# Kernel optimization log

Measured on AMD Instinct MI355X. Metric: run time of the kernel, lower is better.

## Reference

```python
import jax, jax.numpy as jnp
import numpy as np

NPOINT = 2048
RADIUS = 0.1
NSAMPLE = 32


def fps(xyz, npoint):
    # Furthest point sampling, deterministic start at index 0 (matches pointnet2_utils).
    B, N, _ = xyz.shape
    dist0 = jnp.full((B, N), 1e10, dtype=xyz.dtype)
    far0 = jnp.zeros((B,), dtype=jnp.int32)

    def step(carry, _):
        dist, far = carry
        centroid = jnp.take_along_axis(xyz, far[:, None, None], axis=1)  # (B,1,3)
        d = jnp.sum((xyz - centroid) ** 2, axis=-1)                      # (B,N)
        dist = jnp.minimum(dist, d)
        new_far = jnp.argmax(dist, axis=-1).astype(jnp.int32)
        return (dist, new_far), far

    _, idx = jax.lax.scan(step, (dist0, far0), None, length=npoint)
    return idx.T  # (B, npoint)


def ball_query(xyz, new_xyz, radius, nsample):
    # For each center, indices of up to nsample points within radius (pad with first hit).
    N = xyz.shape[1]
    sqr = jnp.sum((new_xyz[:, :, None, :] - xyz[:, None, :, :]) ** 2, axis=-1)  # (B,S,N)
    cand = jnp.where(sqr <= radius * radius, jnp.arange(N, dtype=jnp.int32), N)
    cand = jnp.sort(cand, axis=-1)[:, :, :nsample]  # (B,S,K)
    first = cand[:, :, :1]
    first = jnp.where(first == N, 0, first)
    return jnp.where(cand == N, first, cand)


def batched_gather(points, idx):
    # points (B,N,C), idx (B,...) -> (B,...,C)
    return jax.vmap(lambda p, i: p[i])(points, idx)


def reference(xyz, features, W0, b0, W1, b1, W2, b2):
    # xyz: (B,N,3), features: (B,C,N)
    fps_idx = fps(xyz, NPOINT)                                  # (B,S)
    new_xyz = batched_gather(xyz, fps_idx)                      # (B,S,3)
    idx = ball_query(xyz, new_xyz, RADIUS, NSAMPLE)             # (B,S,K)

    grouped_xyz = batched_gather(xyz, idx) - new_xyz[:, :, None, :]   # (B,S,K,3) relative coords
    grouped_feat = batched_gather(features.transpose(0, 2, 1), idx)   # (B,S,K,C)
    grouped = jnp.concatenate([grouped_xyz, grouped_feat], axis=-1)   # (B,S,K,C+3)
    x = grouped.transpose(0, 3, 1, 2)                                 # (B,C+3,S,K)

    # SharedMLP: 1x1 conv2d + ReLU stack
    x = jax.nn.relu(jnp.einsum('oi,bisk->bosk', W0, x) + b0[None, :, None, None])
    x = jax.nn.relu(jnp.einsum('oi,bisk->bosk', W1, x) + b1[None, :, None, None])
    x = jax.nn.relu(jnp.einsum('oi,bisk->bosk', W2, x) + b2[None, :, None, None])

    new_features = jnp.max(x, axis=-1)  # max-pool over nsample -> (B,128,S)
    return new_xyz, new_features


def setup_inputs() -> dict:
    key = jax.random.key(0)
    ks = jax.random.split(key, 8)
    B, N, C = 4, 8192, 64
    s = 0.05  # keep activations in a sane range through 3 relu layers
    return {
        'xyz': jax.random.uniform(ks[0], (B, N, 3), dtype=jnp.float32),
        'features': jax.random.normal(ks[1], (B, C, N), dtype=jnp.float32),
        'W0': jax.random.normal(ks[2], (64, 67), dtype=jnp.float32) * s,
        'b0': jax.random.normal(ks[3], (64,), dtype=jnp.float32) * s,
        'W1': jax.random.normal(ks[4], (64, 64), dtype=jnp.float32) * s,
        'b1': jax.random.normal(ks[5], (64,), dtype=jnp.float32) * s,
        'W2': jax.random.normal(ks[6], (128, 64), dtype=jnp.float32) * s,
        'b2': jax.random.normal(ks[7], (128,), dtype=jnp.float32) * s,
    }
```

## Files before the change

### kernel.cpp

```cpp
#include <hip/hip_runtime.h>

#define NB 4
#define NPTS 8192
#define NPOINT 2048
#define NSAMPLE 32
#define CF 64
#define CIN 67
#define G 8

typedef float f32x2 __attribute__((ext_vector_type(2)));
typedef unsigned long long u64;

__device__ __forceinline__ f32x2 pk_add(f32x2 a, f32x2 b) {
  f32x2 d;
  asm("v_pk_add_f32 %0, %1, %2" : "=v"(d) : "v"(a), "v"(b));
  return d;
}
__device__ __forceinline__ f32x2 pk_mul(f32x2 a, f32x2 b) {
  f32x2 d;
  asm("v_pk_mul_f32 %0, %1, %2" : "=v"(d) : "v"(a), "v"(b));
  return d;
}

template <int CTRL, int RM>
__device__ __forceinline__ int dppi(int v) {
  return __builtin_amdgcn_update_dpp(0, v, CTRL, RM, 0xf, true);
}
template <int CTRL, int RM>
__device__ __forceinline__ u64 kstep(u64 k) {
  unsigned lo = (unsigned)k, hi = (unsigned)(k >> 32);
  unsigned olo = (unsigned)dppi<CTRL, RM>((int)lo);
  unsigned ohi = (unsigned)dppi<CTRL, RM>((int)hi);
  u64 o = ((u64)ohi << 32) | olo;
  return o > k ? o : k;
}
__device__ __forceinline__ u64 wave_max_key(u64 key) {
  key = kstep<0x111, 0xf>(key);
  key = kstep<0x112, 0xf>(key);
  key = kstep<0x114, 0xf>(key);
  key = kstep<0x118, 0xf>(key);
  key = kstep<0x142, 0xa>(key);
  key = kstep<0x143, 0xc>(key);
  return key;
}
__device__ __forceinline__ unsigned wave_scan_incl(unsigned v) {
  v += (unsigned)__builtin_amdgcn_update_dpp(0, (int)v, 0x111, 0xf, 0xf, true);
  v += (unsigned)__builtin_amdgcn_update_dpp(0, (int)v, 0x112, 0xf, 0xf, true);
  v += (unsigned)__builtin_amdgcn_update_dpp(0, (int)v, 0x114, 0xf, 0xf, true);
  v += (unsigned)__builtin_amdgcn_update_dpp(0, (int)v, 0x118, 0xf, 0xf, true);
  v += (unsigned)__builtin_amdgcn_update_dpp(0, (int)v, 0x142, 0xa, 0xf, true);
  v += (unsigned)__builtin_amdgcn_update_dpp(0, (int)v, 0x143, 0xc, 0xf, true);
  return v;
}

__device__ __forceinline__ int cellof(float x) {
  int c = (int)(x * 8.0f);
  return c > 7 ? 7 : (c < 0 ? 0 : c);
}
__device__ __forceinline__ unsigned morton9(int ix, int iy, int iz) {
  unsigned m = 0;
#pragma unroll
  for (int k = 0; k < 3; ++k) {
    m |= ((unsigned)((ix >> k) & 1) << (3 * k + 2)) |
         ((unsigned)((iy >> k) & 1) << (3 * k + 1)) |
         ((unsigned)((iz >> k) & 1) << (3 * k + 0));
  }
  return m;
}

__global__ __launch_bounds__(512) void fps_kernel(const float* __restrict__ xyz,
                                                  float* __restrict__ new_xyz) {
  const int b = blockIdx.x;
  const int tid = threadIdx.x;
  const int lane = tid & 63;
  const int wid = tid >> 6;
  __shared__ float sx[NPTS], sy[NPTS], sz[NPTS];
  __shared__ unsigned sidx[NPTS];
  __shared__ unsigned offs[512];
  __shared__ unsigned wsum[8];
  __shared__ int farhist[NPOINT];
  __shared__ __align__(16) u64 skey[2][8];

  const float* xb = xyz + (size_t)b * NPTS * 3;
  for (int i = tid; i < NPTS; i += 512) {
    sx[i] = xb[3 * i + 0];
    sy[i] = xb[3 * i + 1];
    sz[i] = xb[3 * i + 2];
  }
  offs[tid] = 0;
  __syncthreads();
  for (int r = 0; r < 16; ++r) {
    int i = tid + r * 512;
    unsigned m = morton9(cellof(sx[i]), cellof(sy[i]), cellof(sz[i]));
    atomicAdd(&offs[m], 1u);
  }
  __syncthreads();
  unsigned v = offs[tid];
  unsigned inc = wave_scan_incl(v);
  if (lane == 63) wsum[wid] = inc;
  __syncthreads();
  unsigned pre = 0;
#pragma unroll
  for (int w = 0; w < 8; ++w) pre += (w < wid) ? wsum[w] : 0u;
  unsigned excl = pre + inc - v;
  __syncthreads();
  offs[tid] = excl;
  __syncthreads();
  for (int r = 0; r < 16; ++r) {
    int i = tid + r * 512;
    unsigned m = morton9(cellof(sx[i]), cellof(sy[i]), cellof(sz[i]));
    unsigned pos = atomicAdd(&offs[m], 1u);
    sidx[pos] = (unsigned)i;
  }
  __syncthreads();

  f32x2 px[8], py[8], pz[8];
  float dist[16];
  unsigned noid[16];
  float blx = 1e30f, bhx = -1e30f, bly = 1e30f, bhy = -1e30f,
        blz = 1e30f, bhz = -1e30f;
#pragma unroll
  for (int j = 0; j < 8; ++j) {
    unsigned i0 = sidx[tid * 16 + 2 * j], i1 = sidx[tid * 16 + 2 * j + 1];
    noid[2 * j] = ~i0; noid[2 * j + 1] = ~i1;
    float x0 = sx[i0], x1 = sx[i1];
    float y0 = sy[i0], y1 = sy[i1];
    float z0 = sz[i0], z1 = sz[i1];
    px[j].x = x0; px[j].y = x1;
    py[j].x = y0; py[j].y = y1;
    pz[j].x = z0; pz[j].y = z1;
    blx = fminf(blx, fminf(x0, x1)); bhx = fmaxf(bhx, fmaxf(x0, x1));
    bly = fminf(bly, fminf(y0, y1)); bhy = fmaxf(bhy, fmaxf(y0, y1));
    blz = fminf(blz, fminf(z0, z1)); bhz = fmaxf(bhz, fmaxf(z0, z1));
    dist[2 * j] = 1e10f; dist[2 * j + 1] = 1e10f;
  }
  float gmaxd = 1e30f;
  u64 gkey = 0;
  int far = 0;
  for (int it = 0; it < NPOINT; ++it) {
    if (tid == 0) farhist[it] = far;
    const float cx = sx[far], cy = sy[far], cz = sz[far];
    float gx = fmaxf(fmaxf(blx - cx, cx - bhx), 0.f);
    float gy = fmaxf(fmaxf(bly - cy, cy - bhy), 0.f);
    float gz = fmaxf(fmaxf(blz - cz, cz - bhz), 0.f);
    float mind2 = gx * gx + gy * gy + gz * gz;
    if (mind2 * 0.999f < gmaxd) {
      f32x2 ncx, ncy, ncz;
      ncx.x = -cx; ncx.y = -cx;
      ncy.x = -cy; ncy.y = -cy;
      ncz.x = -cz; ncz.y = -cz;
      u64 k = 0;
#pragma unroll
      for (int j = 0; j < 8; ++j) {
        f32x2 dx = pk_add(px[j], ncx);
        f32x2 dy = pk_add(py[j], ncy);
        f32x2 dz = pk_add(pz[j], ncz);
        f32x2 xx = pk_mul(dx, dx);
        f32x2 yy = pk_mul(dy, dy);
        f32x2 dd = pk_add(pk_add(xx, yy), pk_mul(dz, dz));
        float n0 = fminf(dist[2 * j], dd.x);
        float n1 = fminf(dist[2 * j + 1], dd.y);
        dist[2 * j] = n0; dist[2 * j + 1] = n1;
        u64 k0 = ((u64)__float_as_uint(n0) << 32) | noid[2 * j];
        k = k0 > k ? k0 : k;
        u64 k1 = ((u64)__float_as_uint(n1) << 32) | noid[2 * j + 1];
        k = k1 > k ? k1 : k;
      }
      gkey = k;
      gmaxd = __uint_as_float((unsigned)(k >> 32));
    }
    u64 key = wave_max_key(gkey);
    const int p = it & 1;
    if (lane == 63) skey[p][wid] = key;
    __syncthreads();
    const ulonglong2* kp = (const ulonglong2*)&skey[p][0];
    ulonglong2 k0 = kp[0], k1 = kp[1], k2 = kp[2], k3 = kp[3];
    u64 m0 = k0.x > k0.y ? k0.x : k0.y;
    u64 m1 = k1.x > k1.y ? k1.x : k1.y;
    u64 m2 = k2.x > k2.y ? k2.x : k2.y;
    u64 m3 = k3.x > k3.y ? k3.x : k3.y;
    u64 m4 = m0 > m1 ? m0 : m1;
    u64 m5 = m2 > m3 ? m2 : m3;
    u64 best = m4 > m5 ? m4 : m5;
    far = (int)~(unsigned)best;
  }
  __syncthreads();
  for (int t = tid; t < NPOINT; t += 512) {
    int f = farhist[t];
    float* o = new_xyz + ((size_t)b * NPOINT + t) * 3;
    o[0] = sx[f]; o[1] = sy[f]; o[2] = sz[f];
  }
}

__global__ __launch_bounds__(256) void tr_kernel(const float* __restrict__ f,
                                                 float* __restrict__ ft) {
  int idx = blockIdx.x * 256 + threadIdx.x;
  int c = idx & 63;
  int i = (idx >> 6) & (NPTS - 1);
  int b = idx >> 19;
  ft[idx] = f[((size_t)(b * CF + c)) * NPTS + i];
}

__global__ __launch_bounds__(256) void bq_kernel(const float* __restrict__ xyz,
                                                 const float* __restrict__ new_xyz,
                                                 int* __restrict__ idxbuf) {
  const int lane = threadIdx.x & 63;
  const int gw = (blockIdx.x * 256 + threadIdx.x) >> 6;
  const int b = gw >> 11;
  const int j = gw & 2047;
  const float* xb = xyz + (size_t)b * NPTS * 3;
  const float* c = new_xyz + ((size_t)b * NPOINT + j) * 3;
  const float cx = c[0], cy = c[1], cz = c[2];
  int* out = idxbuf + ((size_t)b * NPOINT + j) * NSAMPLE;
  const float r2 = 0.01f;
  int found = 0, first = 0;
  for (int base = 0; base < NPTS && found < NSAMPLE; base += 64) {
    const int i = base + lane;
    float dx = xb[3 * i + 0] - cx, dy = xb[3 * i + 1] - cy, dz = xb[3 * i + 2] - cz;
    float d = __fadd_rn(__fadd_rn(__fmul_rn(dx, dx), __fmul_rn(dy, dy)),
                        __fmul_rn(dz, dz));
    bool in = (d <= r2);
    unsigned long long mask = __ballot(in);
    if (mask) {
      if (found == 0) first = base + (__ffsll(mask) - 1);
      int slot = found + __popcll(mask & ((1ull << lane) - 1ull));
      if (in && slot < NSAMPLE) out[slot] = i;
      found += (int)__popcll(mask);
    }
  }
  for (int s = found + lane; s < NSAMPLE; s += 64) out[s] = first;
}

__global__ __launch_bounds__(256) void mlp_kernel(const float* __restrict__ xyz,
                                                  const float* __restrict__ ft,
                                                  const float* __restrict__ feat,
                                                  const int* __restrict__ idxbuf,
                                                  const float* __restrict__ new_xyz,
                                                  const float* __restrict__ W0,
                                                  const float* __restrict__ b0,
                                                  const float* __restrict__ W1,
                                                  const float* __restrict__ b1,
                                                  const float* __restrict__ W2,
                                                  const float* __restrict__ b2,
                                                  float* __restrict__ out_nf,
                                                  int use_ft) {
  __shared__ __align__(16) float Ws0[CIN * 64];
  __shared__ __align__(16) float Ws1[64 * 64];
  __shared__ __align__(16) float Ws2[64 * 128];
  __shared__ float bs0[64], bs1[64], bs2[128];
  __shared__ __align__(16) float X0[CIN * 32];
  __shared__ __align__(16) float X1[64 * 32];
  const int tid = threadIdx.x;
  const int k = tid & 31;
  const int og = tid >> 5;
  for (int t = tid; t < 64 * CIN; t += 256) {
    int o = t / CIN, c = t - o * CIN;
    Ws0[c * 64 + o] = W0[t];
  }
  for (int t = tid; t < 64 * 64; t += 256) Ws1[(t & 63) * 64 + (t >> 6)] = W1[t];
  for (int t = tid; t < 128 * 64; t += 256) Ws2[(t & 63) * 128 + (t >> 6)] = W2[t];
  if (tid < 64) { bs0[tid] = b0[tid]; bs1[tid] = b1[tid]; }
  if (tid < 128) bs2[tid] = b2[tid];
  __syncthreads();

  for (int g = 0; g < G; ++g) {
    const int cj = blockIdx.x * G + g;
    const int b = cj >> 11;
    const int j = cj & 2047;
    const int ni = idxbuf[cj * NSAMPLE + k];
    if (og == 0) {
      const float* ctr = new_xyz + (size_t)cj * 3;
      const float* pp = xyz + ((size_t)b * NPTS + ni) * 3;
      X0[0 * 32 + k] = pp[0] - ctr[0];
      X0[1 * 32 + k] = pp[1] - ctr[1];
      X0[2 * 32 + k] = pp[2] - ctr[2];
    }
    const int cbase = 3 + og * 8;
    if (use_ft) {
      const float4* fr = (const float4*)(ft + ((size_t)b * NPTS + ni) * CF + og * 8);
      float4 f0 = fr[0], f1 = fr[1];
      X0[(cbase + 0) * 32 + k] = f0.x; X0[(cbase + 1) * 32 + k] = f0.y;
      X0[(cbase + 2) * 32 + k] = f0.z; X0[(cbase + 3) * 32 + k] = f0.w;
      X0[(cbase + 4) * 32 + k] = f1.x; X0[(cbase + 5) * 32 + k] = f1.y;
      X0[(cbase + 6) * 32 + k] = f1.z; X0[(cbase + 7) * 32 + k] = f1.w;
    } else {
      const float* fb = feat + (size_t)b * CF * NPTS + ni;
#pragma unroll
      for (int q = 0; q < 8; ++q)
        X0[(cbase + q) * 32 + k] = fb[(size_t)(og * 8 + q) * NPTS];
    }
    __syncthreads();

    float acc[8];
#pragma unroll
    for (int i = 0; i < 8; ++i) acc[i] = bs0[og * 8 + i];
    for (int c = 0; c < CIN; ++c) {
      float xv = X0[c * 32 + k];
      const float4* wr = (const float4*)&Ws0[c * 64 + og * 8];
      float4 w0 = wr[0], w1 = wr[1];
      acc[0] = fmaf(w0.x, xv, acc[0]); acc[1] = fmaf(w0.y, xv, acc[1]);
      acc[2] = fmaf(w0.z, xv, acc[2]); acc[3] = fmaf(w0.w, xv, acc[3]);
      acc[4] = fmaf(w1.x, xv, acc[4]); acc[5] = fmaf(w1.y, xv, acc[5]);
      acc[6] = fmaf(w1.z, xv, acc[6]); acc[7] = fmaf(w1.w, xv, acc[7]);
    }
#pragma unroll
    for (int i = 0; i < 8; ++i) X1[(og * 8 + i) * 32 + k] = fmaxf(acc[i], 0.f);
    __syncthreads();

    float a1[8];
#pragma unroll
    for (int i = 0; i < 8; ++i) a1[i] = bs1[og * 8 + i];
    for (int c = 0; c < 64; ++c) {
      float xv = X1[c * 32 + k];
      const float4* wr = (const float4*)&Ws1[c * 64 + og * 8];
      float4 w0 = wr[0], w1 = wr[1];
      a1[0] = fmaf(w0.x, xv, a1[0]); a1[1] = fmaf(w0.y, xv, a1[1]);
      a1[2] = fmaf(w0.z, xv, a1[2]); a1[3] = fmaf(w0.w, xv, a1[3]);
      a1[4] = fmaf(w1.x, xv, a1[4]); a1[5] = fmaf(w1.y, xv, a1[5]);
      a1[6] = fmaf(w1.z, xv, a1[6]); a1[7] = fmaf(w1.w, xv, a1[7]);
    }
#pragma unroll
    for (int i = 0; i < 8; ++i) X0[(og * 8 + i) * 32 + k] = fmaxf(a1[i], 0.f);
    __syncthreads();

    float a2[16];
#pragma unroll
    for (int i = 0; i < 16; ++i) a2[i] = bs2[og * 16 + i];
    for (int c = 0; c < 64; ++c) {
      float xv = X0[c * 32 + k];
      const float4* wr = (const float4*)&Ws2[c * 128 + og * 16];
      float4 w0 = wr[0], w1 = wr[1], w2 = wr[2], w3 = wr[3];
      a2[0]  = fmaf(w0.x, xv, a2[0]);  a2[1]  = fmaf(w0.y, xv, a2[1]);
      a2[2]  = fmaf(w0.z, xv, a2[2]);  a2[3]  = fmaf(w0.w, xv, a2[3]);
      a2[4]  = fmaf(w1.x, xv, a2[4]);  a2[5]  = fmaf(w1.y, xv, a2[5]);
      a2[6]  = fmaf(w1.z, xv, a2[6]);  a2[7]  = fmaf(w1.w, xv, a2[7]);
      a2[8]  = fmaf(w2.x, xv, a2[8]);  a2[9]  = fmaf(w2.y, xv, a2[9]);
      a2[10] = fmaf(w2.z, xv, a2[10]); a2[11] = fmaf(w2.w, xv, a2[11]);
      a2[12] = fmaf(w3.x, xv, a2[12]); a2[13] = fmaf(w3.y, xv, a2[13]);
      a2[14] = fmaf(w3.z, xv, a2[14]); a2[15] = fmaf(w3.w, xv, a2[15]);
    }
#pragma unroll
    for (int i = 0; i < 16; ++i) {
      float v = fmaxf(a2[i], 0.f);
#pragma unroll
      for (int m = 1; m < 32; m <<= 1) v = fmaxf(v, __shfl_xor(v, m));
      a2[i] = v;
    }
    if (k == 0) {
#pragma unroll
      for (int i = 0; i < 16; ++i)
        out_nf[((size_t)b * 128 + og * 16 + i) * NPOINT + j] = a2[i];
    }
    __syncthreads();
  }
}

extern "C" void kernel_launch(void* const* d_in, const int* in_sizes, int n_in,
                              void* d_out, int out_size, void* d_ws, size_t ws_size,
                              hipStream_t stream) {
  (void)in_sizes; (void)n_in; (void)out_size;
  const float* xyz  = (const float*)d_in[0];
  const float* feat = (const float*)d_in[1];
  const float* W0   = (const float*)d_in[2];
  const float* b0   = (const float*)d_in[3];
  const float* W1   = (const float*)d_in[4];
  const float* b1   = (const float*)d_in[5];
  const float* W2   = (const float*)d_in[6];
  const float* b2   = (const float*)d_in[7];
  float* new_xyz = (float*)d_out;
  float* out_nf  = (float*)d_out + (size_t)NB * NPOINT * 3;

  int* idxbuf = (int*)d_ws;
  size_t idx_bytes = (size_t)NB * NPOINT * NSAMPLE * sizeof(int);
  float* ft = (float*)((char*)d_ws + idx_bytes);
  size_t need = idx_bytes + (size_t)NB * NPTS * CF * sizeof(float);
  int use_ft = (ws_size >= need) ? 1 : 0;

  fps_kernel<<<NB, 512, 0, stream>>>(xyz, new_xyz);
  if (use_ft) tr_kernel<<<(NB * NPTS * CF) / 256, 256, 0, stream>>>(feat, ft);
  bq_kernel<<<(NB * NPOINT) / 4, 256, 0, stream>>>(xyz, new_xyz, idxbuf);
  mlp_kernel<<<(NB * NPOINT) / G, 256, 0, stream>>>(xyz, ft, feat, idxbuf, new_xyz,
                                                    W0, b0, W1, b1, W2, b2,
                                                    out_nf, use_ft);
}
```

Before: 2.133 ms.

## Store FPS points in Morton-sorted LDS arrays and reload them each iteration

```diff
diff --git a/kernel.cpp b/kernel.cpp
--- a/kernel.cpp
+++ b/kernel.cpp
@@ -8,19 +8,7 @@
 #define CIN 67
 #define G 8
 
-typedef float f32x2 __attribute__((ext_vector_type(2)));
 typedef unsigned long long u64;
-
-__device__ __forceinline__ f32x2 pk_add(f32x2 a, f32x2 b) {
-  f32x2 d;
-  asm("v_pk_add_f32 %0, %1, %2" : "=v"(d) : "v"(a), "v"(b));
-  return d;
-}
-__device__ __forceinline__ f32x2 pk_mul(f32x2 a, f32x2 b) {
-  f32x2 d;
-  asm("v_pk_mul_f32 %0, %1, %2" : "=v"(d) : "v"(a), "v"(b));
-  return d;
-}
 
 template <int CTRL, int RM>
 __device__ __forceinline__ int dppi(int v) {
@@ -74,25 +62,21 @@
   const int tid = threadIdx.x;
   const int lane = tid & 63;
   const int wid = tid >> 6;
-  __shared__ float sx[NPTS], sy[NPTS], sz[NPTS];
-  __shared__ unsigned sidx[NPTS];
+  __shared__ __align__(16) float sxs[NPTS], sys[NPTS], szs[NPTS];
+  __shared__ __align__(16) unsigned sidx[NPTS];
   __shared__ unsigned offs[512];
   __shared__ unsigned wsum[8];
   __shared__ int farhist[NPOINT];
   __shared__ __align__(16) u64 skey[2][8];
+  __shared__ int spos0;
 
   const float* xb = xyz + (size_t)b * NPTS * 3;
-  for (int i = tid; i < NPTS; i += 512) {
-    sx[i] = xb[3 * i + 0];
-    sy[i] = xb[3 * i + 1];
-    sz[i] = xb[3 * i + 2];
-  }
   offs[tid] = 0;
   __syncthreads();
   for (int r = 0; r < 16; ++r) {
     int i = tid + r * 512;
-    unsigned m = morton9(cellof(sx[i]), cellof(sy[i]), cellof(sz[i]));
-    atomicAdd(&offs[m], 1u);
+    float x = xb[3 * i + 0], y = xb[3 * i + 1], z = xb[3 * i + 2];
+    atomicAdd(&offs[morton9(cellof(x), cellof(y), cellof(z))], 1u);
   }
   __syncthreads();
   unsigned v = offs[tid];
@@ -108,66 +92,77 @@
   __syncthreads();
   for (int r = 0; r < 16; ++r) {
     int i = tid + r * 512;
-    unsigned m = morton9(cellof(sx[i]), cellof(sy[i]), cellof(sz[i]));
+    float x = xb[3 * i + 0], y = xb[3 * i + 1], z = xb[3 * i + 2];
+    unsigned m = morton9(cellof(x), cellof(y), cellof(z));
     unsigned pos = atomicAdd(&offs[m], 1u);
-    sidx[pos] = (unsigned)i;
-  }
-  __syncthreads();
-
-  f32x2 px[8], py[8], pz[8];
-  float dist[16];
-  unsigned noid[16];
+    sxs[pos] = x; sys[pos] = y; szs[pos] = z; sidx[pos] = (unsigned)i;
+    if (i == 0) spos0 = (int)pos;
+  }
+  __syncthreads();
+
+  const int base = tid * 16;
   float blx = 1e30f, bhx = -1e30f, bly = 1e30f, bhy = -1e30f,
         blz = 1e30f, bhz = -1e30f;
-#pragma unroll
-  for (int j = 0; j < 8; ++j) {
-    unsigned i0 = sidx[tid * 16 + 2 * j], i1 = sidx[tid * 16 + 2 * j + 1];
-    noid[2 * j] = ~i0; noid[2 * j + 1] = ~i1;
-    float x0 = sx[i0], x1 = sx[i1];
-    float y0 = sy[i0], y1 = sy[i1];
-    float z0 = sz[i0], z1 = sz[i1];
-    px[j].x = x0; px[j].y = x1;
-    py[j].x = y0; py[j].y = y1;
-    pz[j].x = z0; pz[j].y = z1;
-    blx = fminf(blx, fminf(x0, x1)); bhx = fmaxf(bhx, fmaxf(x0, x1));
-    bly = fminf(bly, fminf(y0, y1)); bhy = fmaxf(bhy, fmaxf(y0, y1));
-    blz = fminf(blz, fminf(z0, z1)); bhz = fmaxf(bhz, fmaxf(z0, z1));
-    dist[2 * j] = 1e10f; dist[2 * j + 1] = 1e10f;
-  }
+  {
+    const float4* x4 = (const float4*)&sxs[base];
+    const float4* y4 = (const float4*)&sys[base];
+    const float4* z4 = (const float4*)&szs[base];
+#pragma unroll
+    for (int q = 0; q < 4; ++q) {
+      float4 xv = x4[q], yv = y4[q], zv = z4[q];
+      blx = fminf(blx, fminf(fminf(xv.x, xv.y), fminf(xv.z, xv.w)));
+      bhx = fmaxf(bhx, fmaxf(fmaxf(xv.x, xv.y), fmaxf(xv.z, xv.w)));
+      bly = fminf(bly, fminf(fminf(yv.x, yv.y), fminf(yv.z, yv.w)));
+      bhy = fmaxf(bhy, fmaxf(fmaxf(yv.x, yv.y), fmaxf(yv.z, yv.w)));
+      blz = fminf(blz, fminf(fminf(zv.x, zv.y), fminf(zv.z, zv.w)));
+      bhz = fmaxf(bhz, fmaxf(fmaxf(zv.x, zv.y), fmaxf(zv.z, zv.w)));
+    }
+  }
+  float dist[16];
+#pragma unroll
+  for (int j = 0; j < 16; ++j) dist[j] = 1e10f;
+
   float gmaxd = 1e30f;
   u64 gkey = 0;
-  int far = 0;
+  int far = spos0;
   for (int it = 0; it < NPOINT; ++it) {
     if (tid == 0) farhist[it] = far;
-    const float cx = sx[far], cy = sy[far], cz = sz[far];
+    const float cx = sxs[far], cy = sys[far], cz = szs[far];
     float gx = fmaxf(fmaxf(blx - cx, cx - bhx), 0.f);
     float gy = fmaxf(fmaxf(bly - cy, cy - bhy), 0.f);
     float gz = fmaxf(fmaxf(blz - cz, cz - bhz), 0.f);
     float mind2 = gx * gx + gy * gy + gz * gz;
     if (mind2 * 0.999f < gmaxd) {
-      f32x2 ncx, ncy, ncz;
-      ncx.x = -cx; ncx.y = -cx;
-      ncy.x = -cy; ncy.y = -cy;
-      ncz.x = -cz; ncz.y = -cz;
+      const float4* x4 = (const float4*)&sxs[base];
+      const float4* y4 = (const float4*)&sys[base];
+      const float4* z4 = (const float4*)&szs[base];
+      const uint4* i4 = (const uint4*)&sidx[base];
       u64 k = 0;
 #pragma unroll
-      for (int j = 0; j < 8; ++j) {
-        f32x2 dx = pk_add(px[j], ncx);
-        f32x2 dy = pk_add(py[j], ncy);
-        f32x2 dz = pk_add(pz[j], ncz);
-        f32x2 xx = pk_mul(dx, dx);
-        f32x2 yy = pk_mul(dy, dy);
-        f32x2 dd = pk_add(pk_add(xx, yy), pk_mul(dz, dz));
-        float n0 = fminf(dist[2 * j], dd.x);
-        float n1 = fminf(dist[2 * j + 1], dd.y);
-        dist[2 * j] = n0; dist[2 * j + 1] = n1;
-        u64 k0 = ((u64)__float_as_uint(n0) << 32) | noid[2 * j];
-        k = k0 > k ? k0 : k;
-        u64 k1 = ((u64)__float_as_uint(n1) << 32) | noid[2 * j + 1];
-        k = k1 > k ? k1 : k;
+      for (int q = 0; q < 4; ++q) {
+        float4 xv = x4[q], yv = y4[q], zv = z4[q];
+        uint4 iv = i4[q];
+        const float px[4] = {xv.x, xv.y, xv.z, xv.w};
+        const float py[4] = {yv.x, yv.y, yv.z, yv.w};
+        const float pz[4] = {zv.x, zv.y, zv.z, zv.w};
+        const unsigned pi[4] = {iv.x, iv.y, iv.z, iv.w};
+#pragma unroll
+        for (int t = 0; t < 4; ++t) {
+          const int j = q * 4 + t;
+          float dx = __fsub_rn(px[t], cx);
+          float dy = __fsub_rn(py[t], cy);
+          float dz = __fsub_rn(pz[t], cz);
+          float d = __fadd_rn(__fadd_rn(__fmul_rn(dx, dx), __fmul_rn(dy, dy)),
+                              __fmul_rn(dz, dz));
+          float nd = fminf(dist[j], d);
+          dist[j] = nd;
+          u64 kk = ((u64)__float_as_uint(nd) << 26) |
+                   ((u64)(8191u - pi[t]) << 13) | (unsigned)(base + j);
+          k = kk > k ? kk : k;
+        }
       }
       gkey = k;
-      gmaxd = __uint_as_float((unsigned)(k >> 32));
+      gmaxd = __uint_as_float((unsigned)(gkey >> 26));
     }
     u64 key = wave_max_key(gkey);
     const int p = it & 1;
@@ -182,13 +177,13 @@
     u64 m4 = m0 > m1 ? m0 : m1;
     u64 m5 = m2 > m3 ? m2 : m3;
     u64 best = m4 > m5 ? m4 : m5;
-    far = (int)~(unsigned)best;
+    far = (int)(best & 8191u);
   }
   __syncthreads();
   for (int t = tid; t < NPOINT; t += 512) {
     int f = farhist[t];
     float* o = new_xyz + ((size_t)b * NPOINT + t) * 3;
-    o[0] = sx[f]; o[1] = sy[f]; o[2] = sz[f];
+    o[0] = sxs[f]; o[1] = sys[f]; o[2] = szs[f];
   }
 }
 
```

Result: slower. 2.995 ms (+40.4%).
